# Kernel tuning notes

Hardware: AMD Instinct MI355X
Metric: run time of the kernel (lower is better)

The kernel has to match this reference:

```python
import jax, jax.numpy as jnp
import numpy as np

N_NODES = 50000
N_EDGES = 800000
D_IN = 128
D_OUT = 128
D_RED = 32  # out_features // reduction
ORDER = 3


def setup_inputs() -> dict:
    key = jax.random.key(0)
    ks = jax.random.split(key, 16)
    s = 1.0 / np.sqrt(D_IN)
    inp = {
        'features': jax.random.normal(ks[0], (N_NODES, D_IN), jnp.float32),
        'edge_row': jax.random.randint(ks[1], (N_EDGES,), 0, N_NODES, jnp.int32),
        'edge_col': jax.random.randint(ks[2], (N_EDGES,), 0, N_NODES, jnp.int32),
        'edge_val': jax.random.uniform(ks[3], (N_EDGES,), jnp.float32) / 16.0,  # ~1/avg_degree normalization
        'w1': jax.random.normal(ks[4], (D_IN, D_OUT), jnp.float32) * s,
        'b1': jax.random.normal(ks[5], (D_OUT,), jnp.float32) * s,
        'w2': jax.random.normal(ks[6], (D_IN, D_OUT), jnp.float32) * s,
        'b2': jax.random.normal(ks[7], (D_OUT,), jnp.float32) * s,
        'w3': jax.random.normal(ks[8], (D_IN, D_OUT), jnp.float32) * s,
        'b3': jax.random.normal(ks[9], (D_OUT,), jnp.float32) * s,
        'fc1_w': jax.random.normal(ks[10], (D_OUT, D_RED), jnp.float32) * s,
        'fc1_b': jax.random.normal(ks[11], (D_RED,), jnp.float32) * s,
        'fc2_w': jax.random.normal(ks[12], (D_RED, D_OUT), jnp.float32) * (1.0 / np.sqrt(D_RED)),
        'fc2_b': jax.random.normal(ks[13], (D_OUT,), jnp.float32) * s,
    }
    return inp


def reference(features, edge_row, edge_col, edge_val, w1, b1, w2, b2, w3, b3,
              fc1_w, fc1_b, fc2_w, fc2_b):
    def spmm(x):  # sparse [N,N] @ dense [N,D] via gather + segment_sum
        msgs = edge_val[:, None] * x[edge_col]          # [E, D]
        return jax.ops.segment_sum(msgs, edge_row, num_segments=N_NODES)

    def ngnn(w, b, order):
        h = jnp.tanh(features @ w)                      # active=True path
        for _ in range(order):                          # order spmm hops
            h = spmm(h)
        return h + b

    abstract = [ngnn(w, b, k + 1) for k, (w, b) in enumerate([(w1, b1), (w2, b2), (w3, b3)])]
    feats = jnp.stack(abstract, axis=0)                 # [order, N, D]
    m = jnp.mean(feats, axis=1)                         # [order, D]
    a = jax.nn.relu(m @ fc1_w + fc1_b) @ fc2_w + fc2_b  # [order, D]
    a = jax.nn.softmax(a, axis=0)                       # softmax over order dim
    out = jnp.einsum('ond,od->nd', feats, a)            # weighted combine
    return out
```

## Files before the change

### kernel.cpp

```cpp
#include <hip/hip_runtime.h>
#include <cstdint>

#define N_NODES 50000
#define N_EDGES 800000
#define DIM 128
#define EPCAP 64

typedef _Float16 half8 __attribute__((ext_vector_type(8)));
typedef float f32x4 __attribute__((ext_vector_type(4)));


__device__ inline unsigned pack_half2(float lo, float hi) {
    union { _Float16 h[2]; unsigned u; } cv;
    cv.h[0] = (_Float16)lo; cv.h[1] = (_Float16)hi;
    return cv.u;
}
__device__ inline float h_lo(unsigned u) {
    union { unsigned u; _Float16 h[2]; } cv; cv.u = u; return (float)cv.h[0];
}
__device__ inline float h_hi(unsigned u) {
    union { unsigned u; _Float16 h[2]; } cv; cv.u = u; return (float)cv.h[1];
}


__global__ __launch_bounds__(256) void scatter_wprep_kernel(const int* __restrict__ rows,
                                                            const int* __restrict__ cols,
                                                            const float* __restrict__ vals,
                                                            int* __restrict__ cnt,
                                                            unsigned* __restrict__ ep,
                                                            const float* __restrict__ w3,
                                                            const float* __restrict__ w2,
                                                            const float* __restrict__ w1,
                                                            _Float16* __restrict__ Wt) {
    int bx = blockIdx.x;
    if (bx >= 3125) {
        int b = bx - 3125;
        const float* W = (b == 0) ? w3 : (b == 1) ? w2 : w1;
        _Float16* O = Wt + (size_t)b * 16384;
        for (int i = threadIdx.x; i < 16384; i += 256) {
            int j = i >> 7, d = i & 127;
            O[j * 128 + d] = (_Float16)W[d * 128 + j];
        }
        return;
    }
    int e = bx * 256 + threadIdx.x;
    int r = rows[e];
    int p = atomicAdd(&cnt[r], 1);
    union { _Float16 h; unsigned short s; } cv; cv.h = (_Float16)vals[e];
    if (p < EPCAP)
        __builtin_nontemporal_store(((unsigned)cv.s << 16) | (unsigned)cols[e],
                                    &ep[(size_t)r * EPCAP + p]);
}


__global__ __launch_bounds__(256) void gemm_mfma3_kernel(const float* __restrict__ F,
                                                         const _Float16* __restrict__ Wt,
                                                         unsigned* __restrict__ T1, int nrows) {
    __shared__ _Float16 Fs[64 * 128];
    __shared__ _Float16 Ws[128 * 128];
    int tid = threadIdx.x;
    int lane = tid & 63, wv = tid >> 6;
    int c = lane & 15, g = lane >> 4;
    int rowbase = blockIdx.x * 64;

    for (int i = tid; i < 4096; i += 256) {
        int r = i >> 6;
        int row = rowbase + r; if (row >= nrows) row = nrows - 1;
        float2 fv = ((const float2*)F)[(size_t)row * 64 + (i & 63)];
        *(unsigned*)((char*)Fs + ((i * 4) ^ ((r & 15) << 4))) = pack_half2(fv.x, fv.y);
    }
    __syncthreads();

    half8 afr[4];
    #pragma unroll
    for (int ks = 0; ks < 4; ++ks) {
        int off = (((wv * 16 + c) * 128 + ks * 32 + g * 8) * 2) ^ (c << 4);
        afr[ks] = *(const half8*)((const char*)Fs + off);
    }

    for (int b = 0; b < 3; ++b) {
        const unsigned* WtU = (const unsigned*)(Wt + (size_t)b * 16384);
        for (int i = tid; i < 8192; i += 256) {
            int j = i >> 6;
            *(unsigned*)((char*)Ws + ((i * 4) ^ ((j & 15) << 4))) = WtU[i];
        }
        __syncthreads();

        f32x4 zero = {0.f, 0.f, 0.f, 0.f};
        f32x4 acc[8];
        #pragma unroll
        for (int t = 0; t < 8; ++t) acc[t] = zero;

        #pragma unroll
        for (int ks = 0; ks < 4; ++ks) {
            #pragma unroll
            for (int t = 0; t < 8; ++t) {
                int j = t * 16 + c;
                int off = ((j * 128 + ks * 32 + g * 8) * 2) ^ ((j & 15) << 4);
                half8 bfr = *(const half8*)((const char*)Ws + off);
                acc[t] = __builtin_amdgcn_mfma_f32_16x16x32_f16(afr[ks], bfr, acc[t], 0, 0, 0);
            }
        }

        #pragma unroll
        for (int t = 0; t < 4; ++t) {
            int j = t * 16 + c;
            #pragma unroll
            for (int r = 0; r < 4; ++r) {
                int row = rowbase + wv * 16 + g * 4 + r;
                if (row < nrows)
                    T1[(size_t)row * 192 + j * 3 + b] =
                        pack_half2(tanhf(acc[t][r]), tanhf(acc[t + 4][r]));
            }
        }
        __syncthreads();
    }
}


template <int NCHUNK, bool F32FINAL>
__global__ __launch_bounds__(512) void spmm_stage_kernel(const int* __restrict__ cnts,
                                                         const unsigned* __restrict__ ep,
                                                         const unsigned* __restrict__ x,
                                                         unsigned* __restrict__ ob0,
                                                         unsigned* __restrict__ obf,
                                                         float* __restrict__ fout,
                                                         float* __restrict__ csum) {
    __shared__ float cs[128];
    int tid = threadIdx.x;
    if (tid < 128) cs[tid] = 0.f;
    __syncthreads();

    int row = blockIdx.x * 8 + (tid >> 6);
    int lane = tid & 63;
    int n = __builtin_amdgcn_readfirstlane(cnts[row]);
    n = n < EPCAP ? n : EPCAP;
    const unsigned* e0 = ep + (size_t)row * EPCAP;

    float ax[NCHUNK], ay[NCHUNK];
    #pragma unroll
    for (int cc = 0; cc < NCHUNK; ++cc) { ax[cc] = 0.f; ay[cc] = 0.f; }

    const unsigned* xl = x + lane * NCHUNK;
    constexpr int U = 8;
    int i = 0;
    for (; i + U <= n; i += U) {
        unsigned p[U];
        #pragma unroll
        for (int u = 0; u < U; ++u) p[u] = e0[i + u];
        unsigned g[U][NCHUNK];
        #pragma unroll
        for (int u = 0; u < U; ++u) {
            size_t b = (size_t)(p[u] & 0xFFFFu) * (NCHUNK * 64);
            if constexpr (NCHUNK == 3) {
                uint3 v = *(const uint3*)(xl + b);
                g[u][0] = v.x; g[u][1] = v.y; g[u][2] = v.z;
            } else if constexpr (NCHUNK == 2) {
                uint2 v = *(const uint2*)(xl + b);
                g[u][0] = v.x; g[u][1] = v.y;
            } else {
                g[u][0] = xl[b];
            }
        }
        #pragma unroll
        for (int u = 0; u < U; ++u) {
            union { unsigned short s; _Float16 h; } cu; cu.s = (unsigned short)(p[u] >> 16);
            float v = (float)cu.h;
            #pragma unroll
            for (int cc = 0; cc < NCHUNK; ++cc) {
                ax[cc] += v * h_lo(g[u][cc]);
                ay[cc] += v * h_hi(g[u][cc]);
            }
        }
    }
    for (; i < n; ++i) {
        unsigned p = e0[i];
        size_t b = (size_t)(p & 0xFFFFu) * (NCHUNK * 64);
        union { unsigned short s; _Float16 h; } cu; cu.s = (unsigned short)(p >> 16);
        float v = (float)cu.h;
        #pragma unroll
        for (int cc = 0; cc < NCHUNK; ++cc) {
            unsigned gg = xl[b + cc];
            ax[cc] += v * h_lo(gg);
            ay[cc] += v * h_hi(gg);
        }
    }

    if constexpr (NCHUNK == 3) {
        uint2 o;
        o.x = pack_half2(ax[0], ay[0]);
        o.y = pack_half2(ax[1], ay[1]);
        *(uint2*)(ob0 + (size_t)row * 128 + lane * 2) = o;
    } else if constexpr (NCHUNK == 2) {
        ob0[(size_t)row * 64 + lane] = pack_half2(ax[0], ay[0]);
    }

    float fx = ax[NCHUNK - 1], fy = ay[NCHUNK - 1];
    if (F32FINAL) {
        fout[(size_t)row * 128 + lane] = fx;
        fout[(size_t)row * 128 + 64 + lane] = fy;
    } else {
        obf[(size_t)row * 64 + lane] = pack_half2(fx, fy);
    }
    atomicAdd(&cs[2 * lane + 0], fx);
    atomicAdd(&cs[2 * lane + 1], fy);
    __syncthreads();
    if (tid < 128) atomicAdd(&csum[(blockIdx.x & 7) * 384 + tid], cs[tid]);
}


__global__ __launch_bounds__(256) void combine_kernel(float* __restrict__ out,
                                                      const unsigned* __restrict__ f2,
                                                      const unsigned* __restrict__ f3,
                                                      const float* __restrict__ csum,
                                                      const float* __restrict__ b1,
                                                      const float* __restrict__ b2,
                                                      const float* __restrict__ b3,
                                                      const float* __restrict__ fc1w,
                                                      const float* __restrict__ fc1b,
                                                      const float* __restrict__ fc2w,
                                                      const float* __restrict__ fc2b) {
    __shared__ float m[3][128];
    __shared__ float rr[3][32];
    __shared__ float wgt[3][128];
    int t = threadIdx.x;

    if (t < 128) {
        const float inv = 1.0f / (float)N_NODES;
        int slot = (t < 64) ? (2 * t) : (2 * (t - 64) + 1);
        #pragma unroll
        for (int k = 0; k < 3; ++k) {
            float s = 0.f;
            #pragma unroll
            for (int rep = 0; rep < 8; ++rep) s += csum[rep * 384 + k * 128 + slot];
            const float* bk = (k == 0) ? b1 : (k == 1) ? b2 : b3;
            m[k][t] = s * inv + bk[t];
        }
    }
    __syncthreads();
    if (t < 96) {
        int k = t >> 5, j = t & 31;
        float acc = fc1b[j];
        for (int d = 0; d < 128; ++d) acc += m[k][d] * fc1w[d * 32 + j];
        rr[k][j] = fmaxf(acc, 0.f);
    }
    __syncthreads();
    if (t < 128) {
        float a[3];
        #pragma unroll
        for (int k = 0; k < 3; ++k) {
            float acc = fc2b[t];
            for (int j = 0; j < 32; ++j) acc += rr[k][j] * fc2w[j * 128 + t];
            a[k] = acc;
        }
        float mx = fmaxf(a[0], fmaxf(a[1], a[2]));
        float e0 = expf(a[0] - mx), e1 = expf(a[1] - mx), e2 = expf(a[2] - mx);
        float s = e0 + e1 + e2;
        wgt[0][t] = e0 / s;
        wgt[1][t] = e1 / s;
        wgt[2][t] = e2 / s;
    }
    __syncthreads();

    const int total = N_NODES * 32;
    int idx0 = blockIdx.x * blockDim.x + threadIdx.x;
    int stride = gridDim.x * blockDim.x;
    int qb = idx0 & 31;
    float4 W0 = *(const float4*)&wgt[0][qb * 4];
    float4 W1 = *(const float4*)&wgt[1][qb * 4];
    float4 W2 = *(const float4*)&wgt[2][qb * 4];
    float4 B1 = ((const float4*)b1)[qb];
    float4 B2 = ((const float4*)b2)[qb];
    float4 B3 = ((const float4*)b3)[qb];
    bool hi = qb >= 16;
    int qm = qb & 15;
    for (int idx = idx0; idx < total; idx += stride) {
        int row = idx >> 5;
        float4 v1 = ((const float4*)out)[idx];
        uint4 u2 = ((const uint4*)f2)[row * 16 + qm];
        uint4 u3 = ((const uint4*)f3)[row * 16 + qm];
        float f2x = hi ? h_hi(u2.x) : h_lo(u2.x);
        float f2y = hi ? h_hi(u2.y) : h_lo(u2.y);
        float f2z = hi ? h_hi(u2.z) : h_lo(u2.z);
        float f2w = hi ? h_hi(u2.w) : h_lo(u2.w);
        float f3x = hi ? h_hi(u3.x) : h_lo(u3.x);
        float f3y = hi ? h_hi(u3.y) : h_lo(u3.y);
        float f3z = hi ? h_hi(u3.z) : h_lo(u3.z);
        float f3w = hi ? h_hi(u3.w) : h_lo(u3.w);
        float4 o;
        o.x = (v1.x + B1.x) * W0.x + (f2x + B2.x) * W1.x + (f3x + B3.x) * W2.x;
        o.y = (v1.y + B1.y) * W0.y + (f2y + B2.y) * W1.y + (f3y + B3.y) * W2.y;
        o.z = (v1.z + B1.z) * W0.z + (f2z + B2.z) * W1.z + (f3z + B3.z) * W2.z;
        o.w = (v1.w + B1.w) * W0.w + (f2w + B2.w) * W1.w + (f3w + B3.w) * W2.w;
        ((float4*)out)[idx] = o;
    }
}


extern "C" void kernel_launch(void* const* d_in, const int* in_sizes, int n_in,
                              void* d_out, int out_size, void* d_ws, size_t ws_size,
                              hipStream_t stream) {
    const float* F    = (const float*)d_in[0];
    const int*   erow = (const int*)d_in[1];
    const int*   ecol = (const int*)d_in[2];
    const float* eval_ = (const float*)d_in[3];
    const float* w1 = (const float*)d_in[4];  const float* b1 = (const float*)d_in[5];
    const float* w2 = (const float*)d_in[6];  const float* b2 = (const float*)d_in[7];
    const float* w3 = (const float*)d_in[8];  const float* b3 = (const float*)d_in[9];
    const float* fc1w = (const float*)d_in[10]; const float* fc1b = (const float*)d_in[11];
    const float* fc2w = (const float*)d_in[12]; const float* fc2b = (const float*)d_in[13];
    float* out = (float*)d_out;

    char* ws = (char*)d_ws;
    size_t off = 0;
    auto alloc = [&](size_t bytes) -> void* {
        off = (off + 255) & ~(size_t)255;
        void* p = ws + off;
        off += bytes;
        return p;
    };
    unsigned* T1   = (unsigned*)alloc((size_t)N_NODES * 192 * 4);
    unsigned* T2   = (unsigned*)alloc((size_t)N_NODES * 128 * 4);
    unsigned* T3   = (unsigned*)alloc((size_t)N_NODES * 64 * 4);
    unsigned* ep   = (unsigned*)alloc((size_t)N_NODES * EPCAP * 4);
    int*   counts  = (int*)alloc((size_t)N_NODES * sizeof(int));
    float* csum    = (float*)alloc(8 * 3 * 128 * sizeof(float));
    _Float16* Wt   = (_Float16*)alloc(3 * 16384 * sizeof(_Float16));
    unsigned* f2bf = T1;
    unsigned* f3bf = T1 + (size_t)N_NODES * 64;

    size_t zlen = (size_t)((char*)csum + 8 * 3 * 128 * sizeof(float) - (char*)counts);
    hipMemsetAsync(counts, 0, zlen, stream);

    scatter_wprep_kernel<<<3125 + 3, 256, 0, stream>>>(erow, ecol, eval_, counts, ep,
                                                       w3, w2, w1, Wt);
    gemm_mfma3_kernel<<<(N_NODES + 63) / 64, 256, 0, stream>>>(F, Wt, T1, N_NODES);

    const int spmmGrid = N_NODES / 8;

    spmm_stage_kernel<3, true><<<spmmGrid, 512, 0, stream>>>(counts, ep, T1, T2,
                                                             nullptr, out, csum + 0 * 128);
    spmm_stage_kernel<2, false><<<spmmGrid, 512, 0, stream>>>(counts, ep, T2, T3,
                                                              f2bf, nullptr, csum + 1 * 128);
    spmm_stage_kernel<1, false><<<spmmGrid, 512, 0, stream>>>(counts, ep, T3, nullptr,
                                                              f3bf, nullptr, csum + 2 * 128);

    combine_kernel<<<2048, 256, 0, stream>>>(out, f2bf, f3bf, csum, b1, b2, b3,
                                             fc1w, fc1b, fc2w, fc2b);
}
```

Baseline: 367.1 us.

## Fuse GEMM into edge-scatter kernel and loop multiple rows per wave in SpMM

Merges the weight-transpose prep, the edge bucketing scatter and the MFMA feature GEMM into one launch. GEMM blocks now read F straight into registers and convert the weights from the original fp32 layout into shared memory, so the Wt intermediate buffer goes away. T1 and T2 change from interleaved per-lane chunks to planar 64-word segments. Each SpMM wave now handles 8 rows serially and accumulates column sums in registers, which removes the shared-memory atomics and the block barrier. Costs: the gathers are narrower scalar loads instead of uint3/uint2, there is less row-level parallelism, and every GEMM block repeats the strided weight conversion.

```diff
diff --git a/kernel.cpp b/kernel.cpp
--- a/kernel.cpp
+++ b/kernel.cpp
@@ -3,7 +3,6 @@
 
 #define N_NODES 50000
 #define N_EDGES 800000
-#define DIM 128
 #define EPCAP 64
 
 typedef _Float16 half8 __attribute__((ext_vector_type(8)));
@@ -23,66 +22,59 @@
 }
 
 
-__global__ __launch_bounds__(256) void scatter_wprep_kernel(const int* __restrict__ rows,
-                                                            const int* __restrict__ cols,
-                                                            const float* __restrict__ vals,
-                                                            int* __restrict__ cnt,
-                                                            unsigned* __restrict__ ep,
-                                                            const float* __restrict__ w3,
-                                                            const float* __restrict__ w2,
-                                                            const float* __restrict__ w1,
-                                                            _Float16* __restrict__ Wt) {
+__global__ __launch_bounds__(256) void pre_kernel(const int* __restrict__ rows,
+                                                  const int* __restrict__ cols,
+                                                  const float* __restrict__ vals,
+                                                  int* __restrict__ cnt,
+                                                  unsigned* __restrict__ ep,
+                                                  const float* __restrict__ F,
+                                                  const float* __restrict__ w3,
+                                                  const float* __restrict__ w2,
+                                                  const float* __restrict__ w1,
+                                                  unsigned* __restrict__ T1) {
+    __shared__ _Float16 Ws[128 * 128];
     int bx = blockIdx.x;
-    if (bx >= 3125) {
-        int b = bx - 3125;
-        const float* W = (b == 0) ? w3 : (b == 1) ? w2 : w1;
-        _Float16* O = Wt + (size_t)b * 16384;
-        for (int i = threadIdx.x; i < 16384; i += 256) {
-            int j = i >> 7, d = i & 127;
-            O[j * 128 + d] = (_Float16)W[d * 128 + j];
-        }
+    int tid = threadIdx.x;
+
+    if (bx < 3125) {
+        int e = bx * 256 + tid;
+        int r = rows[e];
+        int p = atomicAdd(&cnt[r], 1);
+        union { _Float16 h; unsigned short s; } cv; cv.h = (_Float16)vals[e];
+        if (p < EPCAP)
+            __builtin_nontemporal_store(((unsigned)cv.s << 16) | (unsigned)cols[e],
+                                        &ep[(size_t)r * EPCAP + p]);
         return;
     }
-    int e = bx * 256 + threadIdx.x;
-    int r = rows[e];
-    int p = atomicAdd(&cnt[r], 1);
-    union { _Float16 h; unsigned short s; } cv; cv.h = (_Float16)vals[e];
-    if (p < EPCAP)
-        __builtin_nontemporal_store(((unsigned)cv.s << 16) | (unsigned)cols[e],
-                                    &ep[(size_t)r * EPCAP + p]);
-}
-
-
-__global__ __launch_bounds__(256) void gemm_mfma3_kernel(const float* __restrict__ F,
-                                                         const _Float16* __restrict__ Wt,
-                                                         unsigned* __restrict__ T1, int nrows) {
-    __shared__ _Float16 Fs[64 * 128];
-    __shared__ _Float16 Ws[128 * 128];
-    int tid = threadIdx.x;
+
+    int gb = bx - 3125;
     int lane = tid & 63, wv = tid >> 6;
     int c = lane & 15, g = lane >> 4;
-    int rowbase = blockIdx.x * 64;
-
-    for (int i = tid; i < 4096; i += 256) {
-        int r = i >> 6;
-        int row = rowbase + r; if (row >= nrows) row = nrows - 1;
-        float2 fv = ((const float2*)F)[(size_t)row * 64 + (i & 63)];
-        *(unsigned*)((char*)Fs + ((i * 4) ^ ((r & 15) << 4))) = pack_half2(fv.x, fv.y);
-    }
-    __syncthreads();
+    int rowbase = gb * 64;
 
     half8 afr[4];
-    #pragma unroll
-    for (int ks = 0; ks < 4; ++ks) {
-        int off = (((wv * 16 + c) * 128 + ks * 32 + g * 8) * 2) ^ (c << 4);
-        afr[ks] = *(const half8*)((const char*)Fs + off);
+    {
+        int row = rowbase + wv * 16 + c;
+        if (row >= N_NODES) row = N_NODES - 1;
+        const float* fr = F + (size_t)row * 128;
+        #pragma unroll
+        for (int ks = 0; ks < 4; ++ks) {
+            const float4* s4 = (const float4*)(fr + ks * 32 + g * 8);
+            float4 x0 = s4[0], x1 = s4[1];
+            half8 a;
+            a[0] = (_Float16)x0.x; a[1] = (_Float16)x0.y;
+            a[2] = (_Float16)x0.z; a[3] = (_Float16)x0.w;
+            a[4] = (_Float16)x1.x; a[5] = (_Float16)x1.y;
+            a[6] = (_Float16)x1.z; a[7] = (_Float16)x1.w;
+            afr[ks] = a;
+        }
     }
 
     for (int b = 0; b < 3; ++b) {
-        const unsigned* WtU = (const unsigned*)(Wt + (size_t)b * 16384);
-        for (int i = tid; i < 8192; i += 256) {
-            int j = i >> 6;
-            *(unsigned*)((char*)Ws + ((i * 4) ^ ((j & 15) << 4))) = WtU[i];
+        const float* W = (b == 0) ? w3 : (b == 1) ? w2 : w1;
+        for (int i = tid; i < 16384; i += 256) {
+            int d = i >> 7, j = i & 127;
+            *(_Float16*)((char*)Ws + (((j * 128 + d) * 2) ^ ((j & 15) << 4))) = (_Float16)W[i];
         }
         __syncthreads();
 
@@ -108,8 +100,8 @@
             #pragma unroll
             for (int r = 0; r < 4; ++r) {
                 int row = rowbase + wv * 16 + g * 4 + r;
-                if (row < nrows)
-                    T1[(size_t)row * 192 + j * 3 + b] =
+                if (row < N_NODES)
+                    T1[(size_t)row * 192 + b * 64 + j] =
                         pack_half2(tanhf(acc[t][r]), tanhf(acc[t + 4][r]));
             }
         }
@@ -119,93 +111,92 @@
 
 
 template <int NCHUNK, bool F32FINAL>
-__global__ __launch_bounds__(512) void spmm_stage_kernel(const int* __restrict__ cnts,
+__global__ __launch_bounds__(256) void spmm_stage_kernel(const int* __restrict__ cnts,
                                                          const unsigned* __restrict__ ep,
                                                          const unsigned* __restrict__ x,
                                                          unsigned* __restrict__ ob0,
                                                          unsigned* __restrict__ obf,
                                                          float* __restrict__ fout,
-                                                         float* __restrict__ csum) {
-    __shared__ float cs[128];
-    int tid = threadIdx.x;
-    if (tid < 128) cs[tid] = 0.f;
-    __syncthreads();
-
-    int row = blockIdx.x * 8 + (tid >> 6);
-    int lane = tid & 63;
-    int n = __builtin_amdgcn_readfirstlane(cnts[row]);
-    n = n < EPCAP ? n : EPCAP;
-    const unsigned* e0 = ep + (size_t)row * EPCAP;
-
-    float ax[NCHUNK], ay[NCHUNK];
+                                                         float* __restrict__ csumK) {
+    int lane = threadIdx.x & 63;
+    int wid = blockIdx.x * 4 + (threadIdx.x >> 6);
+    int row0 = wid * 8;
+    const unsigned* xl = x + lane;
+    float csx = 0.f, csy = 0.f;
+
+    int nn[8];
     #pragma unroll
-    for (int cc = 0; cc < NCHUNK; ++cc) { ax[cc] = 0.f; ay[cc] = 0.f; }
-
-    const unsigned* xl = x + lane * NCHUNK;
-    constexpr int U = 8;
-    int i = 0;
-    for (; i + U <= n; i += U) {
-        unsigned p[U];
-        #pragma unroll
-        for (int u = 0; u < U; ++u) p[u] = e0[i + u];
-        unsigned g[U][NCHUNK];
-        #pragma unroll
-        for (int u = 0; u < U; ++u) {
-            size_t b = (size_t)(p[u] & 0xFFFFu) * (NCHUNK * 64);
-            if constexpr (NCHUNK == 3) {
-                uint3 v = *(const uint3*)(xl + b);
-                g[u][0] = v.x; g[u][1] = v.y; g[u][2] = v.z;
-            } else if constexpr (NCHUNK == 2) {
-                uint2 v = *(const uint2*)(xl + b);
-                g[u][0] = v.x; g[u][1] = v.y;
-            } else {
-                g[u][0] = xl[b];
-            }
-        }
-        #pragma unroll
-        for (int u = 0; u < U; ++u) {
-            union { unsigned short s; _Float16 h; } cu; cu.s = (unsigned short)(p[u] >> 16);
+    for (int r = 0; r < 8; ++r) {
+        int row = row0 + r;
+        nn[r] = (row < N_NODES) ? cnts[row] : 0;
+    }
+
+    #pragma unroll 1
+    for (int r = 0; r < 8; ++r) {
+        int row = row0 + r;
+        if (row >= N_NODES) break;
+        int n = __builtin_amdgcn_readfirstlane(nn[r]);
+        n = n < EPCAP ? n : EPCAP;
+        const unsigned* e0 = ep + (size_t)row * EPCAP;
+
+        float ax[NCHUNK], ay[NCHUNK];
+        #pragma unroll
+        for (int cc = 0; cc < NCHUNK; ++cc) { ax[cc] = 0.f; ay[cc] = 0.f; }
+
+        constexpr int U = (NCHUNK == 1) ? 8 : 4;
+        int i = 0;
+        for (; i + U <= n; i += U) {
+            unsigned p[U];
+            #pragma unroll
+            for (int u = 0; u < U; ++u) p[u] = e0[i + u];
+            unsigned gx[U][NCHUNK];
+            #pragma unroll
+            for (int u = 0; u < U; ++u) {
+                unsigned b = (p[u] & 0xFFFFu) * (unsigned)(NCHUNK * 64);
+                #pragma unroll
+                for (int cc = 0; cc < NCHUNK; ++cc) gx[u][cc] = xl[b + cc * 64];
+            }
+            #pragma unroll
+            for (int u = 0; u < U; ++u) {
+                union { unsigned short s; _Float16 h; } cu; cu.s = (unsigned short)(p[u] >> 16);
+                float v = (float)cu.h;
+                #pragma unroll
+                for (int cc = 0; cc < NCHUNK; ++cc) {
+                    ax[cc] += v * h_lo(gx[u][cc]);
+                    ay[cc] += v * h_hi(gx[u][cc]);
+                }
+            }
+        }
+        for (; i < n; ++i) {
+            unsigned p = e0[i];
+            unsigned b = (p & 0xFFFFu) * (unsigned)(NCHUNK * 64);
+            union { unsigned short s; _Float16 h; } cu; cu.s = (unsigned short)(p >> 16);
             float v = (float)cu.h;
             #pragma unroll
             for (int cc = 0; cc < NCHUNK; ++cc) {
-                ax[cc] += v * h_lo(g[u][cc]);
-                ay[cc] += v * h_hi(g[u][cc]);
-            }
-        }
-    }
-    for (; i < n; ++i) {
-        unsigned p = e0[i];
-        size_t b = (size_t)(p & 0xFFFFu) * (NCHUNK * 64);
-        union { unsigned short s; _Float16 h; } cu; cu.s = (unsigned short)(p >> 16);
-        float v = (float)cu.h;
-        #pragma unroll
-        for (int cc = 0; cc < NCHUNK; ++cc) {
-            unsigned gg = xl[b + cc];
-            ax[cc] += v * h_lo(gg);
-            ay[cc] += v * h_hi(gg);
-        }
-    }
-
-    if constexpr (NCHUNK == 3) {
-        uint2 o;
-        o.x = pack_half2(ax[0], ay[0]);
-        o.y = pack_half2(ax[1], ay[1]);
-        *(uint2*)(ob0 + (size_t)row * 128 + lane * 2) = o;
-    } else if constexpr (NCHUNK == 2) {
-        ob0[(size_t)row * 64 + lane] = pack_half2(ax[0], ay[0]);
-    }
-
-    float fx = ax[NCHUNK - 1], fy = ay[NCHUNK - 1];
-    if (F32FINAL) {
-        fout[(size_t)row * 128 + lane] = fx;
-        fout[(size_t)row * 128 + 64 + lane] = fy;
-    } else {
-        obf[(size_t)row * 64 + lane] = pack_half2(fx, fy);
-    }
-    atomicAdd(&cs[2 * lane + 0], fx);
-    atomicAdd(&cs[2 * lane + 1], fy);
-    __syncthreads();
-    if (tid < 128) atomicAdd(&csum[(blockIdx.x & 7) * 384 + tid], cs[tid]);
+                unsigned gg = xl[b + cc * 64];
+                ax[cc] += v * h_lo(gg);
+                ay[cc] += v * h_hi(gg);
+            }
+        }
+
+        #pragma unroll
+        for (int cc = 0; cc < NCHUNK - 1; ++cc)
+            ob0[(size_t)row * ((NCHUNK - 1) * 64) + cc * 64 + lane] = pack_half2(ax[cc], ay[cc]);
+
+        float fx = ax[NCHUNK - 1], fy = ay[NCHUNK - 1];
+        if (F32FINAL) {
+            fout[(size_t)row * 128 + lane] = fx;
+            fout[(size_t)row * 128 + 64 + lane] = fy;
+        } else {
+            obf[(size_t)row * 64 + lane] = pack_half2(fx, fy);
+        }
+        csx += fx;
+        csy += fy;
+    }
+
+    atomicAdd(&csumK[(wid & 7) * 384 + 2 * lane + 0], csx);
+    atomicAdd(&csumK[(wid & 7) * 384 + 2 * lane + 1], csy);
 }
 
 
@@ -325,24 +316,22 @@
     unsigned* ep   = (unsigned*)alloc((size_t)N_NODES * EPCAP * 4);
     int*   counts  = (int*)alloc((size_t)N_NODES * sizeof(int));
     float* csum    = (float*)alloc(8 * 3 * 128 * sizeof(float));
-    _Float16* Wt   = (_Float16*)alloc(3 * 16384 * sizeof(_Float16));
     unsigned* f2bf = T1;
     unsigned* f3bf = T1 + (size_t)N_NODES * 64;
 
     size_t zlen = (size_t)((char*)csum + 8 * 3 * 128 * sizeof(float) - (char*)counts);
     hipMemsetAsync(counts, 0, zlen, stream);
 
-    scatter_wprep_kernel<<<3125 + 3, 256, 0, stream>>>(erow, ecol, eval_, counts, ep,
-                                                       w3, w2, w1, Wt);
-    gemm_mfma3_kernel<<<(N_NODES + 63) / 64, 256, 0, stream>>>(F, Wt, T1, N_NODES);
-
-    const int spmmGrid = N_NODES / 8;
-
-    spmm_stage_kernel<3, true><<<spmmGrid, 512, 0, stream>>>(counts, ep, T1, T2,
+    pre_kernel<<<3125 + 782, 256, 0, stream>>>(erow, ecol, eval_, counts, ep,
+                                               F, w3, w2, w1, T1);
+
+    const int spmmGrid = (N_NODES / 8 + 3) / 4;
+
+    spmm_stage_kernel<3, true><<<spmmGrid, 256, 0, stream>>>(counts, ep, T1, T2,
                                                              nullptr, out, csum + 0 * 128);
-    spmm_stage_kernel<2, false><<<spmmGrid, 512, 0, stream>>>(counts, ep, T2, T3,
+    spmm_stage_kernel<2, false><<<spmmGrid, 256, 0, stream>>>(counts, ep, T2, T3,
                                                               f2bf, nullptr, csum + 1 * 128);
-    spmm_stage_kernel<1, false><<<spmmGrid, 512, 0, stream>>>(counts, ep, T3, nullptr,
+    spmm_stage_kernel<1, false><<<spmmGrid, 256, 0, stream>>>(counts, ep, T3, nullptr,
                                                               f3bf, nullptr, csum + 2 * 128);
 
     combine_kernel<<<2048, 256, 0, stream>>>(out, f2bf, f3bf, csum, b1, b2, b3,
```

New measurement: 404.7 us. 10.3% more time.

## Store feature chunks planar in fp16 and keep first-hop output half precision

Applied to the files above, without the earlier changes.

The GEMM output and SpMM intermediates change from interleaved chunk layout (lane*NCHUNK) to planar layout (chunk*64 + lane). Each gathered neighbor row is now read as separate 4-byte loads per chunk instead of one uint3/uint2 vector load. The first-hop result is also written as packed fp16 into a new buffer rather than fp32 into the output, which roughly halves that write and the combine kernel's read of it. The cost is more gather instructions per edge and extra fp16 rounding on the first branch.

```diff
diff --git a/kernel.cpp b/kernel.cpp
--- a/kernel.cpp
+++ b/kernel.cpp
@@ -3,7 +3,6 @@
 
 #define N_NODES 50000
 #define N_EDGES 800000
-#define DIM 128
 #define EPCAP 64
 
 typedef _Float16 half8 __attribute__((ext_vector_type(8)));
@@ -108,8 +107,8 @@
             #pragma unroll
             for (int r = 0; r < 4; ++r) {
                 int row = rowbase + wv * 16 + g * 4 + r;
-                if (row < nrows)
-                    T1[(size_t)row * 192 + j * 3 + b] =
+                if (row < N_NODES)
+                    T1[(size_t)row * 192 + b * 64 + j] =
                         pack_half2(tanhf(acc[t][r]), tanhf(acc[t + 4][r]));
             }
         }
@@ -118,14 +117,13 @@
 }
 
 
-template <int NCHUNK, bool F32FINAL>
+template <int NCHUNK>
 __global__ __launch_bounds__(512) void spmm_stage_kernel(const int* __restrict__ cnts,
                                                          const unsigned* __restrict__ ep,
                                                          const unsigned* __restrict__ x,
                                                          unsigned* __restrict__ ob0,
                                                          unsigned* __restrict__ obf,
-                                                         float* __restrict__ fout,
-                                                         float* __restrict__ csum) {
+                                                         float* __restrict__ csumK) {
     __shared__ float cs[128];
     int tid = threadIdx.x;
     if (tid < 128) cs[tid] = 0.f;
@@ -141,26 +139,19 @@
     #pragma unroll
     for (int cc = 0; cc < NCHUNK; ++cc) { ax[cc] = 0.f; ay[cc] = 0.f; }
 
-    const unsigned* xl = x + lane * NCHUNK;
+    const unsigned* xl = x + lane;
     constexpr int U = 8;
     int i = 0;
     for (; i + U <= n; i += U) {
         unsigned p[U];
         #pragma unroll
         for (int u = 0; u < U; ++u) p[u] = e0[i + u];
-        unsigned g[U][NCHUNK];
+        unsigned gx[U][NCHUNK];
         #pragma unroll
         for (int u = 0; u < U; ++u) {
-            size_t b = (size_t)(p[u] & 0xFFFFu) * (NCHUNK * 64);
-            if constexpr (NCHUNK == 3) {
-                uint3 v = *(const uint3*)(xl + b);
-                g[u][0] = v.x; g[u][1] = v.y; g[u][2] = v.z;
-            } else if constexpr (NCHUNK == 2) {
-                uint2 v = *(const uint2*)(xl + b);
-                g[u][0] = v.x; g[u][1] = v.y;
-            } else {
-                g[u][0] = xl[b];
-            }
+            unsigned b = (p[u] & 0xFFFFu) * (unsigned)(NCHUNK * 64);
+            #pragma unroll
+            for (int cc = 0; cc < NCHUNK; ++cc) gx[u][cc] = xl[b + cc * 64];
         }
         #pragma unroll
         for (int u = 0; u < U; ++u) {
@@ -168,48 +159,39 @@
             float v = (float)cu.h;
             #pragma unroll
             for (int cc = 0; cc < NCHUNK; ++cc) {
-                ax[cc] += v * h_lo(g[u][cc]);
-                ay[cc] += v * h_hi(g[u][cc]);
+                ax[cc] += v * h_lo(gx[u][cc]);
+                ay[cc] += v * h_hi(gx[u][cc]);
             }
         }
     }
     for (; i < n; ++i) {
         unsigned p = e0[i];
-        size_t b = (size_t)(p & 0xFFFFu) * (NCHUNK * 64);
+        unsigned b = (p & 0xFFFFu) * (unsigned)(NCHUNK * 64);
         union { unsigned short s; _Float16 h; } cu; cu.s = (unsigned short)(p >> 16);
         float v = (float)cu.h;
         #pragma unroll
         for (int cc = 0; cc < NCHUNK; ++cc) {
-            unsigned gg = xl[b + cc];
+            unsigned gg = xl[b + cc * 64];
             ax[cc] += v * h_lo(gg);
             ay[cc] += v * h_hi(gg);
         }
     }
 
-    if constexpr (NCHUNK == 3) {
-        uint2 o;
-        o.x = pack_half2(ax[0], ay[0]);
-        o.y = pack_half2(ax[1], ay[1]);
-        *(uint2*)(ob0 + (size_t)row * 128 + lane * 2) = o;
-    } else if constexpr (NCHUNK == 2) {
-        ob0[(size_t)row * 64 + lane] = pack_half2(ax[0], ay[0]);
-    }
+    #pragma unroll
+    for (int cc = 0; cc < NCHUNK - 1; ++cc)
+        ob0[(size_t)row * ((NCHUNK - 1) * 64) + cc * 64 + lane] = pack_half2(ax[cc], ay[cc]);
 
     float fx = ax[NCHUNK - 1], fy = ay[NCHUNK - 1];
-    if (F32FINAL) {
-        fout[(size_t)row * 128 + lane] = fx;
-        fout[(size_t)row * 128 + 64 + lane] = fy;
-    } else {
-        obf[(size_t)row * 64 + lane] = pack_half2(fx, fy);
-    }
+    obf[(size_t)row * 64 + lane] = pack_half2(fx, fy);
     atomicAdd(&cs[2 * lane + 0], fx);
     atomicAdd(&cs[2 * lane + 1], fy);
     __syncthreads();
-    if (tid < 128) atomicAdd(&csum[(blockIdx.x & 7) * 384 + tid], cs[tid]);
+    if (tid < 128) atomicAdd(&csumK[(blockIdx.x & 7) * 384 + tid], cs[tid]);
 }
 
 
 __global__ __launch_bounds__(256) void combine_kernel(float* __restrict__ out,
+                                                      const unsigned* __restrict__ f1,
                                                       const unsigned* __restrict__ f2,
                                                       const unsigned* __restrict__ f3,
                                                       const float* __restrict__ csum,
@@ -276,9 +258,13 @@
     int qm = qb & 15;
     for (int idx = idx0; idx < total; idx += stride) {
         int row = idx >> 5;
-        float4 v1 = ((const float4*)out)[idx];
+        uint4 u1 = ((const uint4*)f1)[row * 16 + qm];
         uint4 u2 = ((const uint4*)f2)[row * 16 + qm];
         uint4 u3 = ((const uint4*)f3)[row * 16 + qm];
+        float f1x = hi ? h_hi(u1.x) : h_lo(u1.x);
+        float f1y = hi ? h_hi(u1.y) : h_lo(u1.y);
+        float f1z = hi ? h_hi(u1.z) : h_lo(u1.z);
+        float f1w = hi ? h_hi(u1.w) : h_lo(u1.w);
         float f2x = hi ? h_hi(u2.x) : h_lo(u2.x);
         float f2y = hi ? h_hi(u2.y) : h_lo(u2.y);
         float f2z = hi ? h_hi(u2.z) : h_lo(u2.z);
@@ -288,10 +274,10 @@
         float f3z = hi ? h_hi(u3.z) : h_lo(u3.z);
         float f3w = hi ? h_hi(u3.w) : h_lo(u3.w);
         float4 o;
-        o.x = (v1.x + B1.x) * W0.x + (f2x + B2.x) * W1.x + (f3x + B3.x) * W2.x;
-        o.y = (v1.y + B1.y) * W0.y + (f2y + B2.y) * W1.y + (f3y + B3.y) * W2.y;
-        o.z = (v1.z + B1.z) * W0.z + (f2z + B2.z) * W1.z + (f3z + B3.z) * W2.z;
-        o.w = (v1.w + B1.w) * W0.w + (f2w + B2.w) * W1.w + (f3w + B3.w) * W2.w;
+        o.x = (f1x + B1.x) * W0.x + (f2x + B2.x) * W1.x + (f3x + B3.x) * W2.x;
+        o.y = (f1y + B1.y) * W0.y + (f2y + B2.y) * W1.y + (f3y + B3.y) * W2.y;
+        o.z = (f1z + B1.z) * W0.z + (f2z + B2.z) * W1.z + (f3z + B3.z) * W2.z;
+        o.w = (f1w + B1.w) * W0.w + (f2w + B2.w) * W1.w + (f3w + B3.w) * W2.w;
         ((float4*)out)[idx] = o;
     }
 }
@@ -322,12 +308,13 @@
     unsigned* T1   = (unsigned*)alloc((size_t)N_NODES * 192 * 4);
     unsigned* T2   = (unsigned*)alloc((size_t)N_NODES * 128 * 4);
     unsigned* T3   = (unsigned*)alloc((size_t)N_NODES * 64 * 4);
+    unsigned* f1h  = (unsigned*)alloc((size_t)N_NODES * 64 * 4);
     unsigned* ep   = (unsigned*)alloc((size_t)N_NODES * EPCAP * 4);
     int*   counts  = (int*)alloc((size_t)N_NODES * sizeof(int));
     float* csum    = (float*)alloc(8 * 3 * 128 * sizeof(float));
     _Float16* Wt   = (_Float16*)alloc(3 * 16384 * sizeof(_Float16));
-    unsigned* f2bf = T1;
-    unsigned* f3bf = T1 + (size_t)N_NODES * 64;
+    unsigned* f2h  = T1;
+    unsigned* f3h  = T1 + (size_t)N_NODES * 64;
 
     size_t zlen = (size_t)((char*)csum + 8 * 3 * 128 * sizeof(float) - (char*)counts);
     hipMemsetAsync(counts, 0, zlen, stream);
@@ -338,13 +325,10 @@
 
     const int spmmGrid = N_NODES / 8;
 
-    spmm_stage_kernel<3, true><<<spmmGrid, 512, 0, stream>>>(counts, ep, T1, T2,
-                                                             nullptr, out, csum + 0 * 128);
-    spmm_stage_kernel<2, false><<<spmmGrid, 512, 0, stream>>>(counts, ep, T2, T3,
-                                                              f2bf, nullptr, csum + 1 * 128);
-    spmm_stage_kernel<1, false><<<spmmGrid, 512, 0, stream>>>(counts, ep, T3, nullptr,
-                                                              f3bf, nullptr, csum + 2 * 128);
-
-    combine_kernel<<<2048, 256, 0, stream>>>(out, f2bf, f3bf, csum, b1, b2, b3,
+    spmm_stage_kernel<3><<<spmmGrid, 512, 0, stream>>>(counts, ep, T1, T2, f1h, csum + 0 * 128);
+    spmm_stage_kernel<2><<<spmmGrid, 512, 0, stream>>>(counts, ep, T2, T3, f2h, csum + 1 * 128);
+    spmm_stage_kernel<1><<<spmmGrid, 512, 0, stream>>>(counts, ep, T3, nullptr, f3h, csum + 2 * 128);
+
+    combine_kernel<<<2048, 256, 0, stream>>>(out, f1h, f2h, f3h, csum, b1, b2, b3,
                                              fc1w, fc1b, fc2w, fc2b);
 }
```

After: 352.1 us. 4.1% less time.
